# Performance work log

Measured on AMD Instinct MI355X. Metric: run time of the kernel, lower is better.

## Reference

```python
import jax, jax.numpy as jnp
import numpy as np

N = 100000   # nodes
E = 500000   # edges
NS = 64      # scalar (0e) multiplicity
NV = 32      # vector (1o) multiplicity
DIM = NS + 3 * NV  # 160
AVG_NEI = 5.0
INV_SQRT3 = 0.5773502691896258


def setup_inputs() -> dict:
    key = jax.random.key(0)
    ks = jax.random.split(key, 14)
    return {
        "node_feats": jax.random.normal(ks[0], (N, DIM), jnp.float32),
        "node_attrs": jax.random.normal(ks[1], (N, 4), jnp.float32),
        "edge_message": jax.random.normal(ks[2], (E, DIM), jnp.float32),
        "edge_index": jax.random.randint(ks[3], (2, E), 0, N, dtype=jnp.int32),
        # UVU tensor product internal shared weights (one weight per u channel per path)
        "w_tp_00": jax.random.normal(ks[4], (NS,), jnp.float32),  # 0e x 0e -> 0e
        "w_tp_01": jax.random.normal(ks[5], (NS,), jnp.float32),  # 0e x 1o -> 1o
        "w_tp_10": jax.random.normal(ks[6], (NV,), jnp.float32),  # 1o x 0e -> 1o
        "w_tp_11": jax.random.normal(ks[7], (NV,), jnp.float32),  # 1o x 1o -> 0e
        # irreps Linear: tp out has 96x0e + 96x1o -> 96x0e + 32x1o
        "W_lin_s": jax.random.normal(ks[8], (NS + NV, NS + NV), jnp.float32),
        "W_lin_v": jax.random.normal(ks[9], (NS + NV, NV), jnp.float32),
        # FullyConnectedTensorProduct self-connection (uvw, v=1)
        "W_sc_000": jax.random.normal(ks[10], (NS, NS + NV), jnp.float32),
        "W_sc_110": jax.random.normal(ks[11], (NV, NS + NV), jnp.float32),
        "W_sc_011": jax.random.normal(ks[12], (NS, NV), jnp.float32),
        "W_sc_101": jax.random.normal(ks[13], (NV, NV), jnp.float32),
    }


def reference(node_feats, node_attrs, edge_message, edge_index,
              w_tp_00, w_tp_01, w_tp_10, w_tp_11,
              W_lin_s, W_lin_v, W_sc_000, W_sc_110, W_sc_011, W_sc_101):
    edge_dst = edge_index[1]
    # scatter-aggregate edge messages per destination node
    msg = jax.ops.segment_sum(edge_message, edge_dst, num_segments=N)
    msg = msg / jnp.sqrt(AVG_NEI)

    ms = msg[:, :NS]                         # [N, 64] scalars
    mv = msg[:, NS:].reshape(N, NV, 3)       # [N, 32, 3] vectors
    a_s = node_attrs[:, :1]                  # [N, 1]
    a_v = node_attrs[:, 1:]                  # [N, 3]

    # UVU tensor product (msg x attrs), per-channel shared weights
    s00 = ms * a_s * w_tp_00                                            # [N,64] 0e
    s11 = jnp.einsum('nuc,nc->nu', mv, a_v) * INV_SQRT3 * w_tp_11       # [N,32] 0e
    v01 = ms[:, :, None] * a_v[:, None, :] * w_tp_01[None, :, None]     # [N,64,3] 1o
    v10 = mv * a_s[:, :, None] * w_tp_10[None, :, None]                 # [N,32,3] 1o
    tp_s = jnp.concatenate([s00, s11], axis=1)   # [N,96]
    tp_v = jnp.concatenate([v01, v10], axis=1)   # [N,96,3]

    # irreps Linear (block diagonal per l, fan-in normalized)
    inv_fan = 1.0 / jnp.sqrt(jnp.float32(NS + NV))
    lin_s = (tp_s @ W_lin_s) * inv_fan                              # [N,96]
    lin_v = jnp.einsum('nuc,uw->nwc', tp_v, W_lin_v) * inv_fan      # [N,32,3]

    # self-connection: FullyConnectedTensorProduct(node_feats_in, node_attrs)
    xs = node_feats[:, :NS]
    xv = node_feats[:, NS:].reshape(N, NV, 3)
    inv2 = 1.0 / jnp.sqrt(2.0)
    sc_s = ((xs * a_s) @ W_sc_000 / jnp.sqrt(jnp.float32(NS))
            + (jnp.einsum('nuc,nc->nu', xv, a_v) * INV_SQRT3) @ W_sc_110 / jnp.sqrt(jnp.float32(NV))) * inv2
    sc_v = (jnp.einsum('nu,uw,nc->nwc', xs, W_sc_011, a_v) / jnp.sqrt(jnp.float32(NS))
            + jnp.einsum('nuc,uw->nwc', xv * a_s[:, :, None], W_sc_101) / jnp.sqrt(jnp.float32(NV))) * inv2

    h_s = lin_s + sc_s   # [N,96] = 64 scalars + 32 gates
    h_v = lin_v + sc_v   # [N,32,3]

    # gated activation: silu on scalars, sigmoid gates scale the vectors
    out_s = jax.nn.silu(h_s[:, :NS])
    gates = jax.nn.sigmoid(h_s[:, NS:])
    out_v = gates[:, :, None] * h_v
    return jnp.concatenate([out_s, out_v.reshape(N, NV * 3)], axis=1)  # [N,160]
```

## Files before the change

kernel.cpp:

```cpp
#include <hip/hip_runtime.h>

typedef unsigned short u16;
typedef unsigned int u32;

#define Nn 100000
#define Ee 500000
#define DIM 160
#define CAP 48

__device__ __forceinline__ u16 f2bf(float f) {
    u32 i = __float_as_uint(f);
    return (u16)((i + 0x7FFFu + ((i >> 16) & 1u)) >> 16);
}

__device__ __forceinline__ u32 eclamp(int v) {
    u32 e = (u32)v;
    return (e > (u32)(Ee - 1)) ? (u32)(Ee - 1) : e;
}

__global__ __launch_bounds__(256) void hist_fill_k(const int* __restrict__ ei,
                                                   int* __restrict__ cnt,
                                                   int* __restrict__ bucket) {
    int e = blockIdx.x * 256 + threadIdx.x;
    if (e >= Ee) return;
    int dst = ei[Ee + e];
    int pos = atomicAdd(&cnt[dst], 1);
    if (pos < CAP) bucket[(size_t)dst * CAP + pos] = e;
}

__global__ __launch_bounds__(512) void gather_tr_k(const float* __restrict__ em,
                                                   const float* __restrict__ feats,
                                                   const int* __restrict__ bucket,
                                                   const int* __restrict__ cnt,
                                                   u32* __restrict__ mfT) {
    __shared__ u32 tile[160][65];
    int n0 = blockIdx.x * 64;
    int w = threadIdx.x >> 6;
    int lane = threadIdx.x & 63;
    int l32 = lane & 31;
    const float s = 0.4472135954999579f;

    int nfirst = n0 + w * 8;
    int npc = (nfirst < Nn) ? nfirst : (Nn - 1);
    int degC = cnt[npc];
    const int* bC = bucket + (size_t)npc * CAP;
    int4 eeA = *reinterpret_cast<const int4*>(bC);
    int4 eeB = *reinterpret_cast<const int4*>(bC + 4);
    const float* fC = feats + (size_t)npc * DIM;
    float fc0 = fC[lane], fc1 = fC[64 + lane], fc2 = fC[128 + l32];

    for (int i = 0; i < 8; ++i) {
        int col = w * 8 + i;
        int n = n0 + col;
        bool act = (n < Nn);
        int deg = act ? degC : 0;
        if (deg > CAP) deg = CAP;
        int4 curA = eeA, curB = eeB;
        float g0 = act ? fc0 : 0.f;
        float g1 = act ? fc1 : 0.f;
        float g2 = act ? fc2 : 0.f;

        if (i < 7) {
            int n2 = n + 1;
            int n2c = (n2 < Nn) ? n2 : (Nn - 1);
            degC = cnt[n2c];
            const int* bN = bucket + (size_t)n2c * CAP;
            eeA = *reinterpret_cast<const int4*>(bN);
            eeB = *reinterpret_cast<const int4*>(bN + 4);
            const float* fN = feats + (size_t)n2c * DIM;
            fc0 = fN[lane]; fc1 = fN[64 + lane]; fc2 = fN[128 + l32];
        }

        float a0 = 0.f, a1 = 0.f, a2 = 0.f;
        if (deg > 0) {
            u32 e0 = eclamp(curA.x), e1 = eclamp(curA.y);
            u32 e2 = eclamp(curA.z), e3 = eclamp(curA.w);
            float m0 = 1.f;
            float m1 = (1 < deg) ? 1.f : 0.f;
            float m2 = (2 < deg) ? 1.f : 0.f;
            float m3 = (3 < deg) ? 1.f : 0.f;
            const float* p0 = em + (size_t)e0 * DIM;
            const float* p1 = em + (size_t)e1 * DIM;
            const float* p2 = em + (size_t)e2 * DIM;
            const float* p3 = em + (size_t)e3 * DIM;
            if (deg <= 4) {
                float t00 = p0[lane],      t10 = p1[lane],      t20 = p2[lane],      t30 = p3[lane];
                float t01 = p0[64 + lane], t11 = p1[64 + lane], t21 = p2[64 + lane], t31 = p3[64 + lane];
                float t02 = p0[128 + l32], t12 = p1[128 + l32], t22 = p2[128 + l32], t32 = p3[128 + l32];
                a0 = m0 * t00 + m1 * t10 + m2 * t20 + m3 * t30;
                a1 = m0 * t01 + m1 * t11 + m2 * t21 + m3 * t31;
                a2 = m0 * t02 + m1 * t12 + m2 * t22 + m3 * t32;
            } else {
                u32 e4 = eclamp(curB.x), e5 = eclamp(curB.y);
                u32 e6 = eclamp(curB.z), e7 = eclamp(curB.w);
                float m4 = 1.f;
                float m5 = (5 < deg) ? 1.f : 0.f;
                float m6 = (6 < deg) ? 1.f : 0.f;
                float m7 = (7 < deg) ? 1.f : 0.f;
                const float* p4 = em + (size_t)e4 * DIM;
                const float* p5 = em + (size_t)e5 * DIM;
                const float* p6 = em + (size_t)e6 * DIM;
                const float* p7 = em + (size_t)e7 * DIM;
                float t00 = p0[lane],      t10 = p1[lane],      t20 = p2[lane],      t30 = p3[lane];
                float t40 = p4[lane],      t50 = p5[lane],      t60 = p6[lane],      t70 = p7[lane];
                float t01 = p0[64 + lane], t11 = p1[64 + lane], t21 = p2[64 + lane], t31 = p3[64 + lane];
                float t41 = p4[64 + lane], t51 = p5[64 + lane], t61 = p6[64 + lane], t71 = p7[64 + lane];
                float t02 = p0[128 + l32], t12 = p1[128 + l32], t22 = p2[128 + l32], t32 = p3[128 + l32];
                float t42 = p4[128 + l32], t52 = p5[128 + l32], t62 = p6[128 + l32], t72 = p7[128 + l32];
                a0 = (m0 * t00 + m1 * t10 + m2 * t20 + m3 * t30)
                   + (m4 * t40 + m5 * t50 + m6 * t60 + m7 * t70);
                a1 = (m0 * t01 + m1 * t11 + m2 * t21 + m3 * t31)
                   + (m4 * t41 + m5 * t51 + m6 * t61 + m7 * t71);
                a2 = (m0 * t02 + m1 * t12 + m2 * t22 + m3 * t32)
                   + (m4 * t42 + m5 * t52 + m6 * t62 + m7 * t72);
                if (deg > 8) {
                    const int* bt = bucket + (size_t)n * CAP;
                    for (int k = 8; k < deg; k += 4) {
                        int4 ee = *reinterpret_cast<const int4*>(bt + k);
                        u32 q0 = eclamp(ee.x), q1 = eclamp(ee.y);
                        u32 q2 = eclamp(ee.z), q3 = eclamp(ee.w);
                        float u0 = 1.f;
                        float u1 = (k + 1 < deg) ? 1.f : 0.f;
                        float u2 = (k + 2 < deg) ? 1.f : 0.f;
                        float u3 = (k + 3 < deg) ? 1.f : 0.f;
                        const float* q0p = em + (size_t)q0 * DIM;
                        const float* q1p = em + (size_t)q1 * DIM;
                        const float* q2p = em + (size_t)q2 * DIM;
                        const float* q3p = em + (size_t)q3 * DIM;
                        a0 += u0 * q0p[lane] + u1 * q1p[lane]
                            + u2 * q2p[lane] + u3 * q3p[lane];
                        a1 += u0 * q0p[64 + lane] + u1 * q1p[64 + lane]
                            + u2 * q2p[64 + lane] + u3 * q3p[64 + lane];
                        a2 += u0 * q0p[128 + l32] + u1 * q1p[128 + l32]
                            + u2 * q2p[128 + l32] + u3 * q3p[128 + l32];
                    }
                }
            }
        }

        tile[lane][col]      = ((u32)f2bf(a0 * s) << 16) | f2bf(g0);
        tile[64 + lane][col] = ((u32)f2bf(a1 * s) << 16) | f2bf(g1);
        if (lane < 32)
            tile[128 + lane][col] = ((u32)f2bf(a2 * s) << 16) | f2bf(g2);
    }
    __syncthreads();
    int n = n0 + lane;
    if (n < Nn) {
        for (int k = 0; k < 20; ++k) {
            int d = w * 20 + k;
            mfT[d * Nn + n] = tile[d][lane];
        }
    }
}

__global__ __launch_bounds__(256) void prep_weights_k(
    const float* __restrict__ Wls, const float* __restrict__ Wlv,
    const float* __restrict__ W000, const float* __restrict__ W110,
    const float* __restrict__ W011, const float* __restrict__ W101,
    const float* __restrict__ w00, const float* __restrict__ w01,
    const float* __restrict__ w10, const float* __restrict__ w11,
    float* __restrict__ W) {
    int i = blockIdx.x * 256 + threadIdx.x;
    const float inv_fan = 0.10206207261596577f;
    const float IS3 = 0.5773502691896258f;
    if (i < 9216) {
        int u = i / 96;
        float sc = inv_fan * (u < 64 ? w00[u] : IS3 * w11[u - 64]);
        W[i] = Wls[i] * sc;
    } else if (i < 12288) {
        int j = i - 9216; int u = j / 32;
        float sc = inv_fan * (u < 64 ? w01[u] : w10[u - 64]);
        W[i] = Wlv[j] * sc;
    } else if (i < 18432) {
        W[i] = W000[i - 12288] * 0.08838834764831845f;
    } else if (i < 21504) {
        W[i] = W110[i - 18432] * (0.125f * IS3);
    } else if (i < 23552) {
        W[i] = W011[i - 21504] * 0.08838834764831845f;
    } else {
        W[i] = W101[i - 23552] * 0.125f;
    }
}

__device__ __forceinline__ float hi_f(u32 v) { return __uint_as_float(v & 0xFFFF0000u); }
__device__ __forceinline__ float lo_f(u32 v) { return __uint_as_float(v << 16); }

__global__ __launch_bounds__(256) void node_s_k(
    const u32* __restrict__ mfT, const float* __restrict__ attrs,
    const float* __restrict__ W, float* __restrict__ out,
    float* __restrict__ gbuf) {
    __shared__ float st[256][33];
    int wb = blockIdx.y;
    int n0 = blockIdx.x * 256;
    int t = threadIdx.x;
    int n = n0 + t;
    bool active = (n < Nn);
    int nc = active ? n : (Nn - 1);

    const float* Wls  = W;
    const float* W000 = W + 12288;
    const float* W110 = W + 18432;

    float4 a = *reinterpret_cast<const float4*>(attrs + (size_t)nc * 4);
    float a_s = a.x, av0 = a.y, av1 = a.z, av2 = a.w;

    float accU[32], accJ[32];
    #pragma unroll
    for (int w = 0; w < 32; ++w) { accU[w] = 0.f; accJ[w] = 0.f; }

    const float* R1 = Wls + wb * 32;
    const float* R2 = W000 + wb * 32;
    const float* R3 = W110 + wb * 32;

    for (int u = 0; u < 64; ++u) {
        u32 v = mfT[u * Nn + nc];
        float m = hi_f(v);
        float x = lo_f(v);
        const float* r1 = R1 + u * 96;
        const float* r2 = R2 + u * 96;
        #pragma unroll
        for (int w = 0; w < 32; ++w) accU[w] += m * r1[w] + x * r2[w];
    }
    for (int j = 0; j < 32; ++j) {
        int d = (64 + 3 * j) * Nn + nc;
        u32 v0 = mfT[d], v1 = mfT[d + Nn], v2 = mfT[d + 2 * Nn];
        float dv = hi_f(v0) * av0 + hi_f(v1) * av1 + hi_f(v2) * av2;
        float dx = lo_f(v0) * av0 + lo_f(v1) * av1 + lo_f(v2) * av2;
        const float* r1 = R1 + (64 + j) * 96;
        const float* r2 = R3 + j * 96;
        #pragma unroll
        for (int w = 0; w < 32; ++w) accJ[w] += dv * r1[w] + dx * r2[w];
    }

    if (wb < 2) {
        #pragma unroll
        for (int w = 0; w < 32; ++w) {
            float h = a_s * accU[w] + accJ[w];
            st[t][w] = h / (1.f + __expf(-h));
        }
        __syncthreads();
        int off = wb * 32;
        for (int k = 0; k < 32; ++k) {
            int f = k * 256 + t;
            int node = f >> 5, w = f & 31;
            int n2 = n0 + node;
            if (n2 < Nn) out[(size_t)n2 * DIM + off + w] = st[node][w];
        }
    } else {
        #pragma unroll
        for (int w = 0; w < 32; ++w) {
            float h = a_s * accU[w] + accJ[w];
            if (active) gbuf[w * Nn + n] = 1.f / (1.f + __expf(-h));
        }
    }
}

__global__ __launch_bounds__(256) void node_v_k(
    const u32* __restrict__ mfT, const float* __restrict__ attrs,
    const float* __restrict__ W, const float* __restrict__ gbuf,
    float* __restrict__ out) {
    __shared__ float st[256][49];
    int half = blockIdx.y;
    int w0 = half * 16;
    int n0 = blockIdx.x * 256;
    int t = threadIdx.x;
    int n = n0 + t;
    bool active = (n < Nn);
    int nc = active ? n : (Nn - 1);

    const float* Wlv  = W + 9216;
    const float* W011 = W + 21504;
    const float* W101 = W + 23552;

    float4 a = *reinterpret_cast<const float4*>(attrs + (size_t)nc * 4);
    float a_s = a.x;
    float av[3] = {a.y, a.z, a.w};

    float ss[16];
    #pragma unroll
    for (int w = 0; w < 16; ++w) ss[w] = 0.f;
    for (int u = 0; u < 64; ++u) {
        u32 v = mfT[u * Nn + nc];
        float m = hi_f(v);
        float x = lo_f(v);
        const float* r1 = Wlv + u * 32 + w0;
        const float* r2 = W011 + u * 32 + w0;
        #pragma unroll
        for (int w = 0; w < 16; ++w) ss[w] += m * r1[w] + x * r2[w];
    }

    float hj[16][3];
    #pragma unroll
    for (int w = 0; w < 16; ++w) {
        hj[w][0] = 0.f; hj[w][1] = 0.f; hj[w][2] = 0.f;
    }
    for (int j = 0; j < 32; ++j) {
        int d = (64 + 3 * j) * Nn + nc;
        u32 v0 = mfT[d], v1 = mfT[d + Nn], v2 = mfT[d + 2 * Nn];
        float m0 = hi_f(v0), m1 = hi_f(v1), m2 = hi_f(v2);
        float x0 = lo_f(v0), x1 = lo_f(v1), x2 = lo_f(v2);
        const float* r1 = Wlv + (64 + j) * 32 + w0;
        const float* r2 = W101 + j * 32 + w0;
        #pragma unroll
        for (int w = 0; w < 16; ++w) {
            float wv = r1[w], wx = r2[w];
            hj[w][0] += m0 * wv + x0 * wx;
            hj[w][1] += m1 * wv + x1 * wx;
            hj[w][2] += m2 * wv + x2 * wx;
        }
    }

    #pragma unroll
    for (int w = 0; w < 16; ++w) {
        float g = gbuf[(w0 + w) * Nn + nc];
        #pragma unroll
        for (int c = 0; c < 3; ++c) {
            float hv = av[c] * ss[w] + a_s * hj[w][c];
            st[t][w * 3 + c] = g * hv;
        }
    }
    __syncthreads();
    int off = 64 + w0 * 3;
    for (int k = 0; k < 48; ++k) {
        int f = k * 256 + t;
        int node = f / 48;
        int idx = f - node * 48;
        int n2 = n0 + node;
        if (n2 < Nn) out[(size_t)n2 * DIM + off + idx] = st[node][idx];
    }
}

extern "C" void kernel_launch(void* const* d_in, const int* in_sizes, int n_in,
                              void* d_out, int out_size, void* d_ws, size_t ws_size,
                              hipStream_t stream) {
    const float* feats = (const float*)d_in[0];
    const float* attrs = (const float*)d_in[1];
    const float* em    = (const float*)d_in[2];
    const int*   ei    = (const int*)d_in[3];
    const float* w00   = (const float*)d_in[4];
    const float* w01   = (const float*)d_in[5];
    const float* w10   = (const float*)d_in[6];
    const float* w11   = (const float*)d_in[7];
    const float* Wls   = (const float*)d_in[8];
    const float* Wlv   = (const float*)d_in[9];
    const float* W000  = (const float*)d_in[10];
    const float* W110  = (const float*)d_in[11];
    const float* W011  = (const float*)d_in[12];
    const float* W101  = (const float*)d_in[13];

    char* ws = (char*)d_ws;
    int*   bucket = (int*)  (ws);
    int*   cnt    = (int*)  (ws + 19200000);
    u32*   mfT    = (u32*)  (ws + 19600000);
    float* gbuf   = (float*)(ws + 83600000);
    float* W      = (float*)(ws + 96400000);

    hipMemsetAsync(cnt, 0, Nn * sizeof(int), stream);

    hist_fill_k<<<(Ee + 255) / 256, 256, 0, stream>>>(ei, cnt, bucket);

    gather_tr_k<<<(Nn + 63) / 64, 512, 0, stream>>>(em, feats, bucket, cnt, mfT);

    prep_weights_k<<<96, 256, 0, stream>>>(Wls, Wlv, W000, W110, W011, W101,
                                           w00, w01, w10, w11, W);

    node_s_k<<<dim3((Nn + 255) / 256, 3), 256, 0, stream>>>(mfT, attrs, W,
                                                            (float*)d_out, gbuf);

    node_v_k<<<dim3((Nn + 255) / 256, 2), 256, 0, stream>>>(mfT, attrs, W,
                                                            gbuf, (float*)d_out);
}
```

Baseline: 717.7 us.

## Pair-interleave transposed node buffer for 8-byte loads and fold memset into prep kernel

Changes the transposed bf16-pair buffer layout so two adjacent feature rows of the same node sit next to each other. The consumer kernels can then issue 8-byte loads and process two rows per iteration. The gather kernel now handles 32 nodes per block, drops its bounds checks because Nn divides evenly, and writes uint2 stores. The count memset is folded into the weight-prep kernel to remove one launch, which adds a dependency on grid size and assumes Nn is a multiple of 32.

```diff
diff --git a/kernel.cpp b/kernel.cpp
--- a/kernel.cpp
+++ b/kernel.cpp
@@ -33,41 +33,36 @@
                                                    const int* __restrict__ bucket,
                                                    const int* __restrict__ cnt,
                                                    u32* __restrict__ mfT) {
-    __shared__ u32 tile[160][65];
-    int n0 = blockIdx.x * 64;
+    __shared__ u32 tile[160][33];
+    int n0 = blockIdx.x * 32;
     int w = threadIdx.x >> 6;
     int lane = threadIdx.x & 63;
     int l32 = lane & 31;
     const float s = 0.4472135954999579f;
 
-    int nfirst = n0 + w * 8;
-    int npc = (nfirst < Nn) ? nfirst : (Nn - 1);
-    int degC = cnt[npc];
-    const int* bC = bucket + (size_t)npc * CAP;
+    int nfirst = n0 + w * 4;
+    int degC = cnt[nfirst];
+    const int* bC = bucket + (size_t)nfirst * CAP;
     int4 eeA = *reinterpret_cast<const int4*>(bC);
     int4 eeB = *reinterpret_cast<const int4*>(bC + 4);
-    const float* fC = feats + (size_t)npc * DIM;
+    const float* fC = feats + (size_t)nfirst * DIM;
     float fc0 = fC[lane], fc1 = fC[64 + lane], fc2 = fC[128 + l32];
 
-    for (int i = 0; i < 8; ++i) {
-        int col = w * 8 + i;
+    for (int i = 0; i < 4; ++i) {
+        int col = w * 4 + i;
         int n = n0 + col;
-        bool act = (n < Nn);
-        int deg = act ? degC : 0;
+        int deg = degC;
         if (deg > CAP) deg = CAP;
         int4 curA = eeA, curB = eeB;
-        float g0 = act ? fc0 : 0.f;
-        float g1 = act ? fc1 : 0.f;
-        float g2 = act ? fc2 : 0.f;
-
-        if (i < 7) {
+        float g0 = fc0, g1 = fc1, g2 = fc2;
+
+        if (i < 3) {
             int n2 = n + 1;
-            int n2c = (n2 < Nn) ? n2 : (Nn - 1);
-            degC = cnt[n2c];
-            const int* bN = bucket + (size_t)n2c * CAP;
+            degC = cnt[n2];
+            const int* bN = bucket + (size_t)n2 * CAP;
             eeA = *reinterpret_cast<const int4*>(bN);
             eeB = *reinterpret_cast<const int4*>(bN + 4);
-            const float* fN = feats + (size_t)n2c * DIM;
+            const float* fN = feats + (size_t)n2 * DIM;
             fc0 = fN[lane]; fc1 = fN[64 + lane]; fc2 = fN[128 + l32];
         }
 
@@ -144,12 +139,14 @@
             tile[128 + lane][col] = ((u32)f2bf(a2 * s) << 16) | f2bf(g2);
     }
     __syncthreads();
-    int n = n0 + lane;
-    if (n < Nn) {
-        for (int k = 0; k < 20; ++k) {
-            int d = w * 20 + k;
-            mfT[d * Nn + n] = tile[d][lane];
-        }
+    int hw = lane >> 5;
+    for (int k = 0; k < 5; ++k) {
+        int p = w * 10 + k * 2 + hw;
+        int d = 2 * p;
+        uint2 val;
+        val.x = tile[d][l32];
+        val.y = tile[d + 1][l32];
+        *reinterpret_cast<uint2*>(mfT + (size_t)d * Nn + 2 * (n0 + l32)) = val;
     }
 }
 
@@ -159,8 +156,9 @@
     const float* __restrict__ W011, const float* __restrict__ W101,
     const float* __restrict__ w00, const float* __restrict__ w01,
     const float* __restrict__ w10, const float* __restrict__ w11,
-    float* __restrict__ W) {
+    float* __restrict__ W, int* __restrict__ cnt) {
     int i = blockIdx.x * 256 + threadIdx.x;
+    if (i < Nn) cnt[i] = 0;
     const float inv_fan = 0.10206207261596577f;
     const float IS3 = 0.5773502691896258f;
     if (i < 9216) {
@@ -177,7 +175,7 @@
         W[i] = W110[i - 18432] * (0.125f * IS3);
     } else if (i < 23552) {
         W[i] = W011[i - 21504] * 0.08838834764831845f;
-    } else {
+    } else if (i < 24576) {
         W[i] = W101[i - 23552] * 0.125f;
     }
 }
@@ -212,24 +210,30 @@
     const float* R2 = W000 + wb * 32;
     const float* R3 = W110 + wb * 32;
 
-    for (int u = 0; u < 64; ++u) {
-        u32 v = mfT[u * Nn + nc];
-        float m = hi_f(v);
-        float x = lo_f(v);
-        const float* r1 = R1 + u * 96;
-        const float* r2 = R2 + u * 96;
-        #pragma unroll
-        for (int w = 0; w < 32; ++w) accU[w] += m * r1[w] + x * r2[w];
-    }
-    for (int j = 0; j < 32; ++j) {
-        int d = (64 + 3 * j) * Nn + nc;
-        u32 v0 = mfT[d], v1 = mfT[d + Nn], v2 = mfT[d + 2 * Nn];
-        float dv = hi_f(v0) * av0 + hi_f(v1) * av1 + hi_f(v2) * av2;
-        float dx = lo_f(v0) * av0 + lo_f(v1) * av1 + lo_f(v2) * av2;
-        const float* r1 = R1 + (64 + j) * 96;
-        const float* r2 = R3 + j * 96;
-        #pragma unroll
-        for (int w = 0; w < 32; ++w) accJ[w] += dv * r1[w] + dx * r2[w];
+    for (int u = 0; u < 64; u += 2) {
+        uint2 v = *reinterpret_cast<const uint2*>(mfT + (size_t)u * Nn + 2 * nc);
+        float mA = hi_f(v.x), xA = lo_f(v.x);
+        float mB = hi_f(v.y), xB = lo_f(v.y);
+        const float* r1a = R1 + u * 96;
+        const float* r2a = R2 + u * 96;
+        #pragma unroll
+        for (int w = 0; w < 32; ++w)
+            accU[w] += (mA * r1a[w] + xA * r2a[w]) + (mB * r1a[96 + w] + xB * r2a[96 + w]);
+    }
+    for (int j = 0; j < 32; j += 2) {
+        int r0 = 64 + 3 * j;
+        uint2 va = *reinterpret_cast<const uint2*>(mfT + (size_t)r0 * Nn + 2 * nc);
+        uint2 vb = *reinterpret_cast<const uint2*>(mfT + (size_t)(r0 + 2) * Nn + 2 * nc);
+        uint2 vc = *reinterpret_cast<const uint2*>(mfT + (size_t)(r0 + 4) * Nn + 2 * nc);
+        float dvA = hi_f(va.x) * av0 + hi_f(va.y) * av1 + hi_f(vb.x) * av2;
+        float dxA = lo_f(va.x) * av0 + lo_f(va.y) * av1 + lo_f(vb.x) * av2;
+        float dvB = hi_f(vb.y) * av0 + hi_f(vc.x) * av1 + hi_f(vc.y) * av2;
+        float dxB = lo_f(vb.y) * av0 + lo_f(vc.x) * av1 + lo_f(vc.y) * av2;
+        const float* r1A = R1 + (64 + j) * 96;
+        const float* r2A = R3 + j * 96;
+        #pragma unroll
+        for (int w = 0; w < 32; ++w)
+            accJ[w] += (dvA * r1A[w] + dxA * r2A[w]) + (dvB * r1A[96 + w] + dxB * r2A[96 + w]);
     }
 
     if (wb < 2) {
@@ -279,14 +283,15 @@
     float ss[16];
     #pragma unroll
     for (int w = 0; w < 16; ++w) ss[w] = 0.f;
-    for (int u = 0; u < 64; ++u) {
-        u32 v = mfT[u * Nn + nc];
-        float m = hi_f(v);
-        float x = lo_f(v);
+    for (int u = 0; u < 64; u += 2) {
+        uint2 v = *reinterpret_cast<const uint2*>(mfT + (size_t)u * Nn + 2 * nc);
+        float mA = hi_f(v.x), xA = lo_f(v.x);
+        float mB = hi_f(v.y), xB = lo_f(v.y);
         const float* r1 = Wlv + u * 32 + w0;
         const float* r2 = W011 + u * 32 + w0;
         #pragma unroll
-        for (int w = 0; w < 16; ++w) ss[w] += m * r1[w] + x * r2[w];
+        for (int w = 0; w < 16; ++w)
+            ss[w] += (mA * r1[w] + xA * r2[w]) + (mB * r1[32 + w] + xB * r2[32 + w]);
     }
 
     float hj[16][3];
@@ -294,19 +299,24 @@
     for (int w = 0; w < 16; ++w) {
         hj[w][0] = 0.f; hj[w][1] = 0.f; hj[w][2] = 0.f;
     }
-    for (int j = 0; j < 32; ++j) {
-        int d = (64 + 3 * j) * Nn + nc;
-        u32 v0 = mfT[d], v1 = mfT[d + Nn], v2 = mfT[d + 2 * Nn];
-        float m0 = hi_f(v0), m1 = hi_f(v1), m2 = hi_f(v2);
-        float x0 = lo_f(v0), x1 = lo_f(v1), x2 = lo_f(v2);
-        const float* r1 = Wlv + (64 + j) * 32 + w0;
-        const float* r2 = W101 + j * 32 + w0;
+    for (int j = 0; j < 32; j += 2) {
+        int r0 = 64 + 3 * j;
+        uint2 va = *reinterpret_cast<const uint2*>(mfT + (size_t)r0 * Nn + 2 * nc);
+        uint2 vb = *reinterpret_cast<const uint2*>(mfT + (size_t)(r0 + 2) * Nn + 2 * nc);
+        uint2 vc = *reinterpret_cast<const uint2*>(mfT + (size_t)(r0 + 4) * Nn + 2 * nc);
+        float mA0 = hi_f(va.x), mA1 = hi_f(va.y), mA2 = hi_f(vb.x);
+        float xA0 = lo_f(va.x), xA1 = lo_f(va.y), xA2 = lo_f(vb.x);
+        float mB0 = hi_f(vb.y), mB1 = hi_f(vc.x), mB2 = hi_f(vc.y);
+        float xB0 = lo_f(vb.y), xB1 = lo_f(vc.x), xB2 = lo_f(vc.y);
+        const float* r1A = Wlv + (64 + j) * 32 + w0;
+        const float* r2A = W101 + j * 32 + w0;
         #pragma unroll
         for (int w = 0; w < 16; ++w) {
-            float wv = r1[w], wx = r2[w];
-            hj[w][0] += m0 * wv + x0 * wx;
-            hj[w][1] += m1 * wv + x1 * wx;
-            hj[w][2] += m2 * wv + x2 * wx;
+            float wvA = r1A[w], wxA = r2A[w];
+            float wvB = r1A[32 + w], wxB = r2A[32 + w];
+            hj[w][0] += (mA0 * wvA + xA0 * wxA) + (mB0 * wvB + xB0 * wxB);
+            hj[w][1] += (mA1 * wvA + xA1 * wxA) + (mB1 * wvB + xB1 * wxB);
+            hj[w][2] += (mA2 * wvA + xA2 * wxA) + (mB2 * wvB + xB2 * wxB);
         }
     }
 
@@ -355,14 +365,13 @@
     float* gbuf   = (float*)(ws + 83600000);
     float* W      = (float*)(ws + 96400000);
 
-    hipMemsetAsync(cnt, 0, Nn * sizeof(int), stream);
+    prep_weights_k<<<(Nn + 255) / 256, 256, 0, stream>>>(Wls, Wlv, W000, W110, W011,
+                                                         W101, w00, w01, w10, w11,
+                                                         W, cnt);
 
     hist_fill_k<<<(Ee + 255) / 256, 256, 0, stream>>>(ei, cnt, bucket);
 
-    gather_tr_k<<<(Nn + 63) / 64, 512, 0, stream>>>(em, feats, bucket, cnt, mfT);
-
-    prep_weights_k<<<96, 256, 0, stream>>>(Wls, Wlv, W000, W110, W011, W101,
-                                           w00, w01, w10, w11, W);
+    gather_tr_k<<<Nn / 32, 512, 0, stream>>>(em, feats, bucket, cnt, mfT);
 
     node_s_k<<<dim3((Nn + 255) / 256, 3), 256, 0, stream>>>(mfT, attrs, W,
                                                             (float*)d_out, gbuf);
```

New measurement: 735.8 us. 1.03x slower.
